# Kernel optimization log

Hardware: AMD Instinct MI355X
Metric: run time of the kernel (lower is better)

The kernel has to match this reference:

```python
import jax, jax.numpy as jnp
import numpy as np

B, C, N, H, W = 4, 3, 262144, 1024, 1024
HW = H * W
GROUP_COLS = ([0], [1, 2], [1])  # AREA, (GRAY_HEIGHT, VARIANCE_LEVEL), GRAY_HEIGHT


def setup_inputs() -> dict:
    key = jax.random.key(0)
    ks = jax.random.split(key, 10)
    rng = np.random.default_rng(0)
    # parent[i] < i (topological order); root (index 0) points to dummy node N.
    u = rng.random((B, C, N - 1))
    par = (u * np.arange(1, N, dtype=np.float64)).astype(np.int32)
    parent = jnp.asarray(np.concatenate([np.full((B, C, 1), N, np.int32), par], axis=-1))
    # gray-level residue (level(node) - level(parent)) >= 0 for a max-tree
    residue = jax.random.uniform(ks[0], (B, C, N), dtype=jnp.float32) * 8.0
    attrs = jax.random.normal(ks[1], (B, C, N, 3), dtype=jnp.float32)
    pixel_node = jax.random.randint(ks[2], (B, C, HW), 0, N, dtype=jnp.int32)
    # torch init: uniform(-1e-5, 1e-5) weights, bias = 1.0
    W0 = jax.random.uniform(ks[3], (1,), minval=-1e-5, maxval=1e-5, dtype=jnp.float32)
    W1 = jax.random.uniform(ks[4], (2,), minval=-1e-5, maxval=1e-5, dtype=jnp.float32)
    W2 = jax.random.uniform(ks[5], (1,), minval=-1e-5, maxval=1e-5, dtype=jnp.float32)
    b0 = jnp.ones((1,), jnp.float32)
    b1 = jnp.ones((1,), jnp.float32)
    b2 = jnp.ones((1,), jnp.float32)
    return {"attrs": attrs, "residue": residue, "W0": W0, "W1": W1, "W2": W2,
            "b0": b0, "b1": b1, "b2": b2, "parent": parent, "pixel_node": pixel_node}


def _tree_prefix(parent, contrib):
    """f(n) = sum of contrib over n and all its ancestors, via pointer jumping.
    parent: (..., N) int32 in [0, N] (N = dummy root sentinel); contrib: (..., N)."""
    n = contrib.shape[-1]
    acc = jnp.concatenate([contrib, jnp.zeros(contrib.shape[:-1] + (1,), contrib.dtype)], -1)
    ptr = jnp.concatenate([parent, jnp.full(parent.shape[:-1] + (1,), n, parent.dtype)], -1)
    for _ in range(int(np.ceil(np.log2(n + 1)))):
        acc = acc + jnp.take_along_axis(acc, ptr, axis=-1)
        ptr = jnp.take_along_axis(ptr, ptr, axis=-1)
    return acc[..., :n]


def reference(attrs, residue, W0, W1, W2, b0, b1, b2, parent, pixel_node):
    Ws, bs = (W0, W1, W2), (b0, b1, b2)
    outs = []
    for cols, Wg, bg in zip(GROUP_COLS, Ws, bs):
        feats = attrs[..., jnp.array(cols)]              # (B,C,N,Fg)
        s = jax.nn.sigmoid(feats @ Wg + bg)              # per-node score (B,C,N)
        f = _tree_prefix(parent, s * residue)            # connected filter (B,C,N)
        outs.append(jnp.take_along_axis(f, pixel_node, axis=-1))  # (B,C,HW)
    y = jnp.stack(outs, axis=2)                          # (B,C,G,HW)
    return y.reshape(B, C * len(GROUP_COLS), H, W)
```

## Files before the change

kernel.cpp:

```cpp
#include <hip/hip_runtime.h>

#define NNODES 262144
#define HWPIX  1048576
#define BC     12

__device__ __forceinline__ float sigm(float x) {
    return 1.0f / (1.0f + __expf(-x));
}

__device__ __forceinline__ int xcd_swizzle(int orig, int nwg) {
    int q = nwg >> 3;
    return (orig & 7) * q + (orig >> 3);
}

__global__ __launch_bounds__(256) void k_contrib(
    const float* __restrict__ attrs,
    const float* __restrict__ residue,
    const int*   __restrict__ parent,
    const float* __restrict__ W0, const float* __restrict__ W1,
    const float* __restrict__ W2, const float* __restrict__ b0,
    const float* __restrict__ b1, const float* __restrict__ b2,
    float4* __restrict__ contrib)
{
    const float w0 = W0[0], w10 = W1[0], w11 = W1[1], w2 = W2[0];
    const float c0 = b0[0], c1 = b1[0], c2 = b2[0];

    int t = blockIdx.x * blockDim.x + threadIdx.x;
    const float4* a4 = (const float4*)attrs + (size_t)t * 3;
    float4 A = a4[0], Bv = a4[1], Cv = a4[2];
    float4 r  = ((const float4*)residue)[t];
    int4  par = ((const int4*)parent)[t];

    float4 o0, o1, o2, o3;
    o0.x = r.x * sigm(A.x * w0 + c0);
    o0.y = r.x * sigm(A.y * w10 + A.z * w11 + c1);
    o0.z = r.x * sigm(A.y * w2 + c2);
    o0.w = __int_as_float(par.x);
    o1.x = r.y * sigm(A.w * w0 + c0);
    o1.y = r.y * sigm(Bv.x * w10 + Bv.y * w11 + c1);
    o1.z = r.y * sigm(Bv.x * w2 + c2);
    o1.w = __int_as_float(par.y);
    o2.x = r.z * sigm(Bv.z * w0 + c0);
    o2.y = r.z * sigm(Bv.w * w10 + Cv.x * w11 + c1);
    o2.z = r.z * sigm(Bv.w * w2 + c2);
    o2.w = __int_as_float(par.z);
    o3.x = r.w * sigm(Cv.y * w0 + c0);
    o3.y = r.w * sigm(Cv.z * w10 + Cv.w * w11 + c1);
    o3.z = r.w * sigm(Cv.z * w2 + c2);
    o3.w = __int_as_float(par.w);

    float4* dst = contrib + (size_t)t * 4;
    dst[0] = o0; dst[1] = o1; dst[2] = o2; dst[3] = o3;
}

__global__ __launch_bounds__(256) void k_scan_chunk(
    const float4* __restrict__ contrib,
    float4* __restrict__ ftab,
    int lo, int cnt)
{
    int w = xcd_swizzle(blockIdx.x, gridDim.x);
    int bpt = cnt >> 8;
    int bc  = w / bpt;
    int i   = lo + (w % bpt) * 256 + threadIdx.x;
    int bcbase = bc << 18;

    float4 c = contrib[bcbase + i];
    float fx = c.x, fy = c.y, fz = c.z;
    int j = __float_as_int(c.w);
    if (lo == 0) {
        while (j != NNODES) {
            float4 cj = contrib[bcbase + j];
            fx += cj.x; fy += cj.y; fz += cj.z;
            j = __float_as_int(cj.w);
        }
    } else {
        while (j >= lo) {
            float4 cj = contrib[bcbase + j];
            fx += cj.x; fy += cj.y; fz += cj.z;
            j = __float_as_int(cj.w);
        }
        float4 fp = ftab[bcbase + j];
        fx += fp.x; fy += fp.y; fz += fp.z;
    }
    ftab[bcbase + i] = make_float4(fx, fy, fz, 0.0f);
}

__global__ __launch_bounds__(256) void k_gather(
    const float4* __restrict__ f,
    const int*    __restrict__ pixel_node,
    float* __restrict__ out)
{
    int w = xcd_swizzle(blockIdx.x, gridDim.x);
    size_t gp = (size_t)w * 2048 + (size_t)threadIdx.x * 8;
    int bc = (int)(gp >> 20);
    int p  = (int)(gp & (HWPIX - 1));
    const int4* pn4 = (const int4*)(pixel_node + gp);
    int4 pa = pn4[0], pb = pn4[1];
    const float4* fb = f + ((size_t)bc << 18);
    float4 f0 = fb[pa.x], f1 = fb[pa.y], f2 = fb[pa.z], f3 = fb[pa.w];
    float4 f4 = fb[pb.x], f5 = fb[pb.y], f6 = fb[pb.z], f7 = fb[pb.w];
    float* o = out + (size_t)bc * 3 * HWPIX + p;
    *(float4*)(o)                 = make_float4(f0.x, f1.x, f2.x, f3.x);
    *(float4*)(o + 4)             = make_float4(f4.x, f5.x, f6.x, f7.x);
    *(float4*)(o + HWPIX)         = make_float4(f0.y, f1.y, f2.y, f3.y);
    *(float4*)(o + HWPIX + 4)     = make_float4(f4.y, f5.y, f6.y, f7.y);
    *(float4*)(o + 2 * HWPIX)     = make_float4(f0.z, f1.z, f2.z, f3.z);
    *(float4*)(o + 2 * HWPIX + 4) = make_float4(f4.z, f5.z, f6.z, f7.z);
}

extern "C" void kernel_launch(void* const* d_in, const int* in_sizes, int n_in,
                              void* d_out, int out_size, void* d_ws, size_t ws_size,
                              hipStream_t stream) {
    const float* attrs      = (const float*)d_in[0];
    const float* residue    = (const float*)d_in[1];
    const float* W0         = (const float*)d_in[2];
    const float* W1         = (const float*)d_in[3];
    const float* W2         = (const float*)d_in[4];
    const float* b0         = (const float*)d_in[5];
    const float* b1         = (const float*)d_in[6];
    const float* b2         = (const float*)d_in[7];
    const int*   parent     = (const int*)d_in[8];
    const int*   pixel_node = (const int*)d_in[9];
    float* out = (float*)d_out;

    const size_t total_nodes = (size_t)BC * NNODES;
    float4* contrib = (float4*)d_ws;
    float4* ftab    = contrib + total_nodes;

    k_contrib<<<(int)(total_nodes / 4 / 256), 256, 0, stream>>>(
        attrs, residue, parent, W0, W1, W2, b0, b1, b2, contrib);

    {
        int bounds[5] = {0, 4096, 16384, 65536, NNODES};
        for (int k = 0; k < 4; ++k) {
            int lo = bounds[k], cnt = bounds[k + 1] - bounds[k];
            int nblk = cnt / 256 * BC;
            k_scan_chunk<<<nblk, 256, 0, stream>>>(contrib, ftab, lo, cnt);
        }
    }

    k_gather<<<(int)((size_t)BC * HWPIX / 2048), 256, 0, stream>>>(
        ftab, pixel_node, out);
}
```

Baseline: 377.8 us.

## Store tree-prefix table in fp16 and chase multiple nodes per thread

Stores the prefix-sum table as half4 instead of float4, halving its footprint for the random gathers in the scan and pixel-gather kernels. Each scan thread now walks CH independent ancestor chains in lockstep, giving more memory-level parallelism with fewer launched threads. The trade is reduced precision: values up to a few hundred are rounded to fp16, which may exceed tolerance. Lockstep chains also leave threads idle while waiting on the longest chain.

```diff
diff --git a/kernel.cpp b/kernel.cpp
--- a/kernel.cpp
+++ b/kernel.cpp
@@ -3,6 +3,8 @@
 #define NNODES 262144
 #define HWPIX  1048576
 #define BC     12
+
+typedef _Float16 half4 __attribute__((ext_vector_type(4)));
 
 __device__ __forceinline__ float sigm(float x) {
     return 1.0f / (1.0f + __expf(-x));
@@ -53,41 +55,77 @@
     dst[0] = o0; dst[1] = o1; dst[2] = o2; dst[3] = o3;
 }
 
-__global__ __launch_bounds__(256) void k_scan_chunk(
+template<int CH, bool BASE>
+__global__ __launch_bounds__(256) void k_scan(
     const float4* __restrict__ contrib,
-    float4* __restrict__ ftab,
+    half4* __restrict__ ftab,
     int lo, int cnt)
 {
     int w = xcd_swizzle(blockIdx.x, gridDim.x);
-    int bpt = cnt >> 8;
-    int bc  = w / bpt;
-    int i   = lo + (w % bpt) * 256 + threadIdx.x;
-    int bcbase = bc << 18;
+    const int sub = cnt / CH;
+    const int bpt = sub >> 8;
+    int bc = w / bpt;
+    int i0 = lo + (w % bpt) * 256 + threadIdx.x;
+    const float4* C = contrib + ((size_t)bc << 18);
+    half4* F = ftab + ((size_t)bc << 18);
 
-    float4 c = contrib[bcbase + i];
-    float fx = c.x, fy = c.y, fz = c.z;
-    int j = __float_as_int(c.w);
-    if (lo == 0) {
-        while (j != NNODES) {
-            float4 cj = contrib[bcbase + j];
-            fx += cj.x; fy += cj.y; fz += cj.z;
-            j = __float_as_int(cj.w);
+    int   j[CH];
+    float ax[CH], ay[CH], az[CH];
+    #pragma unroll
+    for (int k = 0; k < CH; ++k) {
+        float4 e = C[i0 + k * sub];
+        ax[k] = e.x; ay[k] = e.y; az[k] = e.z;
+        j[k] = __float_as_int(e.w);
+    }
+
+    bool any = false;
+    #pragma unroll
+    for (int k = 0; k < CH; ++k)
+        any |= BASE ? (j[k] != NNODES) : (j[k] >= lo);
+
+    while (any) {
+        float4 e[CH];
+        #pragma unroll
+        for (int k = 0; k < CH; ++k) {
+            bool act = BASE ? (j[k] != NNODES) : (j[k] >= lo);
+            e[k] = C[act ? j[k] : 0];
+        }
+        any = false;
+        #pragma unroll
+        for (int k = 0; k < CH; ++k) {
+            bool act = BASE ? (j[k] != NNODES) : (j[k] >= lo);
+            if (act) {
+                ax[k] += e[k].x; ay[k] += e[k].y; az[k] += e[k].z;
+                j[k] = __float_as_int(e[k].w);
+            }
+            any |= BASE ? (j[k] != NNODES) : (j[k] >= lo);
+        }
+    }
+
+    if (BASE) {
+        #pragma unroll
+        for (int k = 0; k < CH; ++k) {
+            half4 h = {(_Float16)ax[k], (_Float16)ay[k], (_Float16)az[k], (_Float16)0.f};
+            F[i0 + k * sub] = h;
         }
     } else {
-        while (j >= lo) {
-            float4 cj = contrib[bcbase + j];
-            fx += cj.x; fy += cj.y; fz += cj.z;
-            j = __float_as_int(cj.w);
+        half4 fp[CH];
+        #pragma unroll
+        for (int k = 0; k < CH; ++k) fp[k] = F[j[k]];
+        #pragma unroll
+        for (int k = 0; k < CH; ++k) {
+            float fx = ax[k] + (float)fp[k].x;
+            float fy = ay[k] + (float)fp[k].y;
+            float fz = az[k] + (float)fp[k].z;
+            half4 h = {(_Float16)fx, (_Float16)fy, (_Float16)fz, (_Float16)0.f};
+            F[i0 + k * sub] = h;
         }
-        float4 fp = ftab[bcbase + j];
-        fx += fp.x; fy += fp.y; fz += fp.z;
     }
-    ftab[bcbase + i] = make_float4(fx, fy, fz, 0.0f);
 }
 
 __global__ __launch_bounds__(256) void k_gather(
-    const float4* __restrict__ f,
-    const int*    __restrict__ pixel_node,
+    const half4* __restrict__ f,
+    const int*   __restrict__ pixel_node,
     float* __restrict__ out)
 {
     int w = xcd_swizzle(blockIdx.x, gridDim.x);
@@ -96,9 +134,9 @@
     int p  = (int)(gp & (HWPIX - 1));
     const int4* pn4 = (const int4*)(pixel_node + gp);
     int4 pa = pn4[0], pb = pn4[1];
-    const float4* fb = f + ((size_t)bc << 18);
-    float4 f0 = fb[pa.x], f1 = fb[pa.y], f2 = fb[pa.z], f3 = fb[pa.w];
-    float4 f4 = fb[pb.x], f5 = fb[pb.y], f6 = fb[pb.z], f7 = fb[pb.w];
+    const half4* fb = f + ((size_t)bc << 18);
+    half4 f0 = fb[pa.x], f1 = fb[pa.y], f2 = fb[pa.z], f3 = fb[pa.w];
+    half4 f4 = fb[pb.x], f5 = fb[pb.y], f6 = fb[pb.z], f7 = fb[pb.w];
     float* o = out + (size_t)bc * 3 * HWPIX + p;
     *(float4*)(o)                 = make_float4(f0.x, f1.x, f2.x, f3.x);
     *(float4*)(o + 4)             = make_float4(f4.x, f5.x, f6.x, f7.x);
@@ -125,19 +163,15 @@
 
     const size_t total_nodes = (size_t)BC * NNODES;
     float4* contrib = (float4*)d_ws;
-    float4* ftab    = contrib + total_nodes;
+    half4*  ftab    = (half4*)(contrib + total_nodes);
 
     k_contrib<<<(int)(total_nodes / 4 / 256), 256, 0, stream>>>(
         attrs, residue, parent, W0, W1, W2, b0, b1, b2, contrib);
 
-    {
-        int bounds[5] = {0, 4096, 16384, 65536, NNODES};
-        for (int k = 0; k < 4; ++k) {
-            int lo = bounds[k], cnt = bounds[k + 1] - bounds[k];
-            int nblk = cnt / 256 * BC;
-            k_scan_chunk<<<nblk, 256, 0, stream>>>(contrib, ftab, lo, cnt);
-        }
-    }
+    k_scan<1, true ><<< 4096 * BC / 256,          256, 0, stream>>>(contrib, ftab, 0,     4096);
+    k_scan<4, false><<< 12288 / 4 * BC / 256,     256, 0, stream>>>(contrib, ftab, 4096,  12288);
+    k_scan<4, false><<< 49152 / 4 * BC / 256,     256, 0, stream>>>(contrib, ftab, 16384, 49152);
+    k_scan<8, false><<< 196608 / 8 * BC / 256,    256, 0, stream>>>(contrib, ftab, 65536, 196608);
 
     k_gather<<<(int)((size_t)BC * HWPIX / 2048), 256, 0, stream>>>(
         ftab, pixel_node, out);
```

Result: faster. 354.5 us (-6.2%).
